# Kernel tuning notes

Hardware: AMD Instinct MI355X
Metric: run time of the kernel (lower is better)

## Reference

```python
import jax, jax.numpy as jnp
import numpy as np

NUM_HEADS = 16


def setup_inputs() -> dict:
    key = jax.random.key(0)
    ks = jax.random.split(key, 4)
    B, S, H = 2, 2048, 1024
    hidden_states = jax.random.normal(ks[0], (B, S, H), dtype=jnp.float32)
    attention_mask = jnp.zeros((B, 1, 1, S), dtype=jnp.float32)
    scale = 1.0 / np.sqrt(H)
    Wq = jax.random.normal(ks[1], (H, H), dtype=jnp.float32) * scale
    Wk = jax.random.normal(ks[2], (H, H), dtype=jnp.float32) * scale
    Wv = jax.random.normal(ks[3], (H, H), dtype=jnp.float32) * scale
    bq = jnp.zeros((H,), dtype=jnp.float32)
    bk = jnp.zeros((H,), dtype=jnp.float32)
    bv = jnp.zeros((H,), dtype=jnp.float32)
    return {"hidden_states": hidden_states, "attention_mask": attention_mask,
            "Wq": Wq, "bq": bq, "Wk": Wk, "bk": bk, "Wv": Wv, "bv": bv}


def _split_heads(x, B, S):
    # [B, S, H] -> [B, h, S, d]
    return x.reshape(B, S, NUM_HEADS, -1).transpose(0, 2, 1, 3)


def reference(hidden_states, attention_mask, Wq, bq, Wk, bk, Wv, bv):
    B, S, H = hidden_states.shape
    d = H // NUM_HEADS
    q = _split_heads(hidden_states @ Wq + bq, B, S)  # [B,h,S,d]
    k = _split_heads(hidden_states @ Wk + bk, B, S)
    v = _split_heads(hidden_states @ Wv + bv, B, S)

    scores = jnp.einsum('bhqd,bhkd->bhqk', q, k) / jnp.sqrt(jnp.float32(d))
    # causal mask: -inf strictly above diagonal, plus additive pad mask
    i = jnp.arange(S)[:, None]
    j = jnp.arange(S)[None, :]
    causal = jnp.where(j > i, -jnp.inf, 0.0).astype(scores.dtype)  # [S,S]
    scores = scores + attention_mask + causal[None, None, :, :]

    probs = jax.nn.softmax(scores, axis=-1)  # dropout prob = 0.0 -> identity
    context = jnp.einsum('bhqk,bhkd->bhqd', probs, v)  # [B,h,S,d]
    return context.transpose(0, 2, 1, 3).reshape(B, S, H)
```

## Files before the change

kernel.cpp:

```cpp
#include <hip/hip_runtime.h>

typedef __attribute__((ext_vector_type(4))) float f32x4;
typedef __attribute__((ext_vector_type(8))) short bf16x8;

__device__ __forceinline__ ushort f2bf(float f) {
  union { float f; unsigned u; } v; v.f = f;
  unsigned u = v.u;
  return (ushort)((u + 0x7fffu + ((u >> 16) & 1u)) >> 16);
}

__global__ __launch_bounds__(256) void cvt_x(const float* __restrict__ x,
                                             ushort* __restrict__ o) {
  int idx = blockIdx.x * 256 + threadIdx.x;
  float4 v = reinterpret_cast<const float4*>(x)[idx];
  ushort4 r;
  r.x = f2bf(v.x); r.y = f2bf(v.y); r.z = f2bf(v.z); r.w = f2bf(v.w);
  reinterpret_cast<ushort4*>(o)[idx] = r;
}

__global__ __launch_bounds__(256) void wtrans(const float* __restrict__ Wq,
                                              const float* __restrict__ Wk,
                                              const float* __restrict__ Wv,
                                              ushort* __restrict__ WT) {
  __shared__ ushort tile[64 * 65];
  int bx = blockIdx.x;
  int w = bx >> 8;
  int rem = bx & 255;
  int k0 = (rem >> 4) << 6;
  int n0 = (rem & 15) << 6;
  const float* W = (w == 0) ? Wq : (w == 1) ? Wk : Wv;
  int tid = threadIdx.x;
#pragma unroll
  for (int it = 0; it < 16; ++it) {
    int idx = tid + it * 256;
    int r = idx >> 6, c = idx & 63;
    tile[r * 65 + c] = f2bf(W[(k0 + r) * 1024 + n0 + c]);
  }
  __syncthreads();
#pragma unroll
  for (int it = 0; it < 16; ++it) {
    int idx = tid + it * 256;
    int r = idx >> 6, c = idx & 63;
    WT[w * 1048576 + (n0 + r) * 1024 + k0 + c] = tile[c * 65 + r];
  }
}

__global__ __launch_bounds__(256) void qkv_gemm(
    const ushort* __restrict__ Xb, const ushort* __restrict__ WT,
    const float* __restrict__ bq, const float* __restrict__ bk,
    const float* __restrict__ bv, ushort* __restrict__ Qb,
    ushort* __restrict__ Kb, ushort* __restrict__ VT) {
  __shared__ ushort Xs[128 * 72];
  __shared__ ushort Ws[128 * 72];
  int tid = threadIdx.x;
  int wave = tid >> 6, lane = tid & 63, g = lane >> 4, lr = lane & 15;
  int wr = wave >> 1, wc = wave & 1;
  int m0 = blockIdx.x << 7;
  int n0g = blockIdx.y << 7;
  f32x4 acc[4][4];
#pragma unroll
  for (int i = 0; i < 4; ++i)
#pragma unroll
    for (int j = 0; j < 4; ++j) { acc[i][j][0] = 0.f; acc[i][j][1] = 0.f; acc[i][j][2] = 0.f; acc[i][j][3] = 0.f; }

  for (int k0 = 0; k0 < 1024; k0 += 64) {
#pragma unroll
    for (int c = 0; c < 4; ++c) {
      int lin = tid + (c << 8);
      int row = lin >> 3, cc = lin & 7;
      *reinterpret_cast<uint4*>(&Xs[row * 72 + cc * 8]) =
          *reinterpret_cast<const uint4*>(&Xb[(m0 + row) * 1024 + k0 + cc * 8]);
      *reinterpret_cast<uint4*>(&Ws[row * 72 + cc * 8]) =
          *reinterpret_cast<const uint4*>(&WT[(n0g + row) * 1024 + k0 + cc * 8]);
    }
    __syncthreads();
#pragma unroll
    for (int ks = 0; ks < 2; ++ks) {
      bf16x8 a[4], b[4];
#pragma unroll
      for (int mi = 0; mi < 4; ++mi)
        a[mi] = *reinterpret_cast<const bf16x8*>(&Xs[(wr * 64 + mi * 16 + lr) * 72 + ks * 32 + g * 8]);
#pragma unroll
      for (int ni = 0; ni < 4; ++ni)
        b[ni] = *reinterpret_cast<const bf16x8*>(&Ws[(wc * 64 + ni * 16 + lr) * 72 + ks * 32 + g * 8]);
#pragma unroll
      for (int mi = 0; mi < 4; ++mi)
#pragma unroll
        for (int ni = 0; ni < 4; ++ni)
          acc[mi][ni] = __builtin_amdgcn_mfma_f32_16x16x32_bf16(a[mi], b[ni], acc[mi][ni], 0, 0, 0);
    }
    __syncthreads();
  }
  int which = n0g >> 10;
  const float* bias = (which == 0) ? bq : (which == 1) ? bk : bv;
  int nb = (n0g & 1023) + wc * 64;
#pragma unroll
  for (int ni = 0; ni < 4; ++ni) {
    int n = nb + ni * 16 + lr;
    float bb = bias[n];
    int hh = n >> 6, dd = n & 63;
#pragma unroll
    for (int mi = 0; mi < 4; ++mi) {
      int mbase = m0 + wr * 64 + mi * 16 + g * 4;
      int b_ = mbase >> 11, s = mbase & 2047;
      if (which == 2) {
        ushort4 v4;
        v4.x = f2bf(acc[mi][ni][0] + bb);
        v4.y = f2bf(acc[mi][ni][1] + bb);
        v4.z = f2bf(acc[mi][ni][2] + bb);
        v4.w = f2bf(acc[mi][ni][3] + bb);
        *reinterpret_cast<ushort4*>(&VT[((size_t)(b_ * 16 + hh) * 64 + dd) * 2048 + s]) = v4;
      } else {
        ushort* ob = (which == 0) ? Qb : Kb;
#pragma unroll
        for (int r = 0; r < 4; ++r)
          ob[((size_t)(b_ * 16 + hh) * 2048 + s + r) * 64 + dd] = f2bf(acc[mi][ni][r] + bb);
      }
    }
  }
}

struct QTState {
  f32x4 o[4];
  float m[4], l[4];
};

__device__ __forceinline__ void attn_process(
    const ushort* Ks, const ushort* VsT, ushort* Psw,
    const bf16x8& aq0, const bf16x8& aq1, QTState& st,
    int g, int lr, int qw, int kv0, bool diag, const float* mv) {
  f32x4 sc[4];
#pragma unroll
  for (int sub = 0; sub < 4; ++sub) {
    f32x4 s;
    s[0] = 0.f; s[1] = 0.f; s[2] = 0.f; s[3] = 0.f;
    bf16x8 bk0 = *reinterpret_cast<const bf16x8*>(&Ks[(sub * 16 + lr) * 72 + g * 8]);
    bf16x8 bk1 = *reinterpret_cast<const bf16x8*>(&Ks[(sub * 16 + lr) * 72 + 32 + g * 8]);
    s = __builtin_amdgcn_mfma_f32_16x16x32_bf16(aq0, bk0, s, 0, 0, 0);
    s = __builtin_amdgcn_mfma_f32_16x16x32_bf16(aq1, bk1, s, 0, 0, 0);
    int kk = kv0 + sub * 16 + lr;
#pragma unroll
    for (int r = 0; r < 4; ++r) {
      float v = s[r] * 0.125f + mv[sub];
      if (diag) {
        int q = qw + g * 4 + r;
        v = (kk > q) ? -__builtin_inff() : v;
      }
      s[r] = v;
    }
    sc[sub] = s;
  }
  float alpha[4];
#pragma unroll
  for (int r = 0; r < 4; ++r) {
    float tm = fmaxf(fmaxf(sc[0][r], sc[1][r]), fmaxf(sc[2][r], sc[3][r]));
    tm = fmaxf(tm, __shfl_xor(tm, 1));
    tm = fmaxf(tm, __shfl_xor(tm, 2));
    tm = fmaxf(tm, __shfl_xor(tm, 4));
    tm = fmaxf(tm, __shfl_xor(tm, 8));
    float nm = fmaxf(st.m[r], tm);
    float al = __expf(st.m[r] - nm);
    float rs = 0.f;
#pragma unroll
    for (int sub = 0; sub < 4; ++sub) {
      float p = __expf(sc[sub][r] - nm);
      sc[sub][r] = p;
      rs += p;
    }
    rs += __shfl_xor(rs, 1);
    rs += __shfl_xor(rs, 2);
    rs += __shfl_xor(rs, 4);
    rs += __shfl_xor(rs, 8);
    st.l[r] = st.l[r] * al + rs;
    st.m[r] = nm;
    alpha[r] = al;
#pragma unroll
    for (int sub = 0; sub < 4; ++sub)
      Psw[(g * 4 + r) * 72 + sub * 16 + lr] = f2bf(sc[sub][r]);
  }
#pragma unroll
  for (int ns = 0; ns < 4; ++ns) {
#pragma unroll
    for (int r = 0; r < 4; ++r) st.o[ns][r] *= alpha[r];
  }
#pragma unroll
  for (int kc = 0; kc < 2; ++kc) {
    bf16x8 pa = *reinterpret_cast<const bf16x8*>(&Psw[lr * 72 + kc * 32 + g * 8]);
#pragma unroll
    for (int ds_ = 0; ds_ < 4; ++ds_) {
      bf16x8 vb = *reinterpret_cast<const bf16x8*>(&VsT[(ds_ * 16 + lr) * 72 + kc * 32 + g * 8]);
      st.o[ds_] = __builtin_amdgcn_mfma_f32_16x16x32_bf16(pa, vb, st.o[ds_], 0, 0, 0);
    }
  }
}

__global__ __launch_bounds__(256) void attn(const ushort* __restrict__ Qb,
                                            const ushort* __restrict__ Kb,
                                            const ushort* __restrict__ VT,
                                            const float* __restrict__ mask,
                                            float* __restrict__ out) {
  __shared__ ushort Ks[64 * 72];
  __shared__ ushort VsT[64 * 72];
  __shared__ ushort Ps[4][16 * 72];
  int tid = threadIdx.x;
  int wave = tid >> 6, lane = tid & 63, g = lane >> 4, lr = lane & 15;
  int pi = blockIdx.x, bh = blockIdx.y;
  int b_ = bh >> 4, h = bh & 15;
  int qa_t = pi, qb_t = 31 - pi;
  const ushort* Qh = Qb + (size_t)bh * 2048 * 64;
  const ushort* Kh = Kb + (size_t)bh * 2048 * 64;
  const ushort* VTh = VT + (size_t)bh * 64 * 2048;
  int qa_w = qa_t * 64 + wave * 16;
  int qb_w = qb_t * 64 + wave * 16;

  bf16x8 aqa0 = *reinterpret_cast<const bf16x8*>(&Qh[(qa_w + lr) * 64 + g * 8]);
  bf16x8 aqa1 = *reinterpret_cast<const bf16x8*>(&Qh[(qa_w + lr) * 64 + 32 + g * 8]);
  bf16x8 aqb0 = *reinterpret_cast<const bf16x8*>(&Qh[(qb_w + lr) * 64 + g * 8]);
  bf16x8 aqb1 = *reinterpret_cast<const bf16x8*>(&Qh[(qb_w + lr) * 64 + 32 + g * 8]);

  QTState sa, sb;
#pragma unroll
  for (int i = 0; i < 4; ++i) {
    sa.o[i][0] = 0.f; sa.o[i][1] = 0.f; sa.o[i][2] = 0.f; sa.o[i][3] = 0.f;
    sb.o[i][0] = 0.f; sb.o[i][1] = 0.f; sb.o[i][2] = 0.f; sb.o[i][3] = 0.f;
    sa.m[i] = -__builtin_inff(); sa.l[i] = 0.f;
    sb.m[i] = -__builtin_inff(); sb.l[i] = 0.f;
  }
  ushort* Psw = Ps[wave];

  for (int t = 0; t <= qb_t; ++t) {
    int kv0 = t << 6;
#pragma unroll
    for (int c = 0; c < 2; ++c) {
      int lin = tid + (c << 8);
      int row = lin >> 3, cc = lin & 7;
      *reinterpret_cast<uint4*>(&Ks[row * 72 + cc * 8]) =
          *reinterpret_cast<const uint4*>(&Kh[(kv0 + row) * 64 + cc * 8]);
      *reinterpret_cast<uint4*>(&VsT[row * 72 + cc * 8]) =
          *reinterpret_cast<const uint4*>(&VTh[row * 2048 + kv0 + cc * 8]);
    }
    float mv[4];
#pragma unroll
    for (int sub = 0; sub < 4; ++sub) mv[sub] = mask[b_ * 2048 + kv0 + sub * 16 + lr];
    __syncthreads();
    if (t <= qa_t)
      attn_process(Ks, VsT, Psw, aqa0, aqa1, sa, g, lr, qa_w, kv0, t == qa_t, mv);
    attn_process(Ks, VsT, Psw, aqb0, aqb1, sb, g, lr, qb_w, kv0, t == qb_t, mv);
    __syncthreads();
  }

#pragma unroll
  for (int ns = 0; ns < 4; ++ns) {
#pragma unroll
    for (int r = 0; r < 4; ++r) {
      int qa = qa_w + g * 4 + r;
      out[(size_t)(b_ * 2048 + qa) * 1024 + h * 64 + ns * 16 + lr] = sa.o[ns][r] / sa.l[r];
      int qb = qb_w + g * 4 + r;
      out[(size_t)(b_ * 2048 + qb) * 1024 + h * 64 + ns * 16 + lr] = sb.o[ns][r] / sb.l[r];
    }
  }
}

extern "C" void kernel_launch(void* const* d_in, const int* in_sizes, int n_in,
                              void* d_out, int out_size, void* d_ws, size_t ws_size,
                              hipStream_t stream) {
  const float* X    = (const float*)d_in[0];
  const float* mask = (const float*)d_in[1];
  const float* Wq   = (const float*)d_in[2];
  const float* bq   = (const float*)d_in[3];
  const float* Wk   = (const float*)d_in[4];
  const float* bk   = (const float*)d_in[5];
  const float* Wv   = (const float*)d_in[6];
  const float* bv   = (const float*)d_in[7];
  float* out = (float*)d_out;

  char* ws = (char*)d_ws;
  ushort* Xb  = (ushort*)ws;
  ushort* WTb = (ushort*)(ws + 8388608);
  ushort* Qb  = (ushort*)(ws + 8388608 + 6291456);
  ushort* Kb  = Qb + 4194304;
  ushort* VT  = Kb + 4194304;

  cvt_x<<<4096, 256, 0, stream>>>(X, Xb);
  wtrans<<<768, 256, 0, stream>>>(Wq, Wk, Wv, WTb);
  qkv_gemm<<<dim3(32, 24), 256, 0, stream>>>(Xb, WTb, bq, bk, bv, Qb, Kb, VT);
  attn<<<dim3(16, 32), 256, 0, stream>>>(Qb, Kb, VT, mask, out);
}
```

Before: 218.4 us.

## Rewrite attention with 32x32 MFMA, register-resident P, and LDS-staged GEMM epilogue

The attention kernel now gives each wave 32 query rows, handled with 32x32x16 MFMAs in transposed form. The probabilities stay in registers via v_cvt_pk_bf16 and permlane32_swap instead of a round trip through LDS. It also swizzles K and V in LDS, skips the rescale when the max rises by less than a threshold, and stages the output through LDS for coalesced float4 stores. The QKV GEMM loads tiles with global_load_lds, uses setprio around its MFMAs, and writes its epilogue through LDS for vectorized stores. These changes target LDS traffic, bank conflicts and scattered stores, at the cost of more complexity and reliance on gfx950-specific instructions.

```diff
diff --git a/kernel.cpp b/kernel.cpp
--- a/kernel.cpp
+++ b/kernel.cpp
@@ -1,12 +1,29 @@
 #include <hip/hip_runtime.h>
 
-typedef __attribute__((ext_vector_type(4))) float f32x4;
-typedef __attribute__((ext_vector_type(8))) short bf16x8;
+typedef __attribute__((ext_vector_type(4)))  float f32x4;
+typedef __attribute__((ext_vector_type(16))) float f32x16;
+typedef __attribute__((ext_vector_type(8)))  short bf16x8;
+
+typedef __attribute__((address_space(1))) const void gvoid;
+typedef __attribute__((address_space(3))) void lvoid;
+
+__device__ __forceinline__ void gl_lds16(const void* g, void* l) {
+  __builtin_amdgcn_global_load_lds((gvoid*)g, (lvoid*)l, 16, 0, 0);
+}
 
 __device__ __forceinline__ ushort f2bf(float f) {
   union { float f; unsigned u; } v; v.f = f;
   unsigned u = v.u;
   return (ushort)((u + 0x7fffu + ((u >> 16) & 1u)) >> 16);
+}
+
+__device__ __forceinline__ uint cvt_pk_bf16(float lo, float hi) {
+  uint r;
+  asm("v_cvt_pk_bf16_f32 %0, %1, %2" : "=v"(r) : "v"(lo), "v"(hi));
+  return r;
+}
+__device__ __forceinline__ void plswap(uint& x, uint& y) {
+  asm volatile("v_permlane32_swap_b32 %0, %1" : "+v"(x), "+v"(y));
 }
 
 __global__ __launch_bounds__(256) void cvt_x(const float* __restrict__ x,
@@ -50,8 +67,9 @@
     const float* __restrict__ bq, const float* __restrict__ bk,
     const float* __restrict__ bv, ushort* __restrict__ Qb,
     ushort* __restrict__ Kb, ushort* __restrict__ VT) {
-  __shared__ ushort Xs[128 * 72];
-  __shared__ ushort Ws[128 * 72];
+  __shared__ ushort smem[128 * 136];
+  ushort* Xs = smem;
+  ushort* Ws = smem + 8192;
   int tid = threadIdx.x;
   int wave = tid >> 6, lane = tid & 63, g = lane >> 4, lr = lane & 15;
   int wr = wave >> 1, wc = wave & 1;
@@ -63,15 +81,15 @@
 #pragma unroll
     for (int j = 0; j < 4; ++j) { acc[i][j][0] = 0.f; acc[i][j][1] = 0.f; acc[i][j][2] = 0.f; acc[i][j][3] = 0.f; }
 
+  int lrow = lane >> 3, lcol = (lane & 7) * 8;
   for (int k0 = 0; k0 < 1024; k0 += 64) {
+    __syncthreads();
 #pragma unroll
     for (int c = 0; c < 4; ++c) {
-      int lin = tid + (c << 8);
-      int row = lin >> 3, cc = lin & 7;
-      *reinterpret_cast<uint4*>(&Xs[row * 72 + cc * 8]) =
-          *reinterpret_cast<const uint4*>(&Xb[(m0 + row) * 1024 + k0 + cc * 8]);
-      *reinterpret_cast<uint4*>(&Ws[row * 72 + cc * 8]) =
-          *reinterpret_cast<const uint4*>(&WT[(n0g + row) * 1024 + k0 + cc * 8]);
+      int cw = wave * 4 + c;
+      int row = cw * 8 + lrow;
+      gl_lds16(Xb + (size_t)(m0 + row) * 1024 + k0 + lcol, Xs + cw * 512);
+      gl_lds16(WT + (size_t)(n0g + row) * 1024 + k0 + lcol, Ws + cw * 512);
     }
     __syncthreads();
 #pragma unroll
@@ -79,117 +97,75 @@
       bf16x8 a[4], b[4];
 #pragma unroll
       for (int mi = 0; mi < 4; ++mi)
-        a[mi] = *reinterpret_cast<const bf16x8*>(&Xs[(wr * 64 + mi * 16 + lr) * 72 + ks * 32 + g * 8]);
+        a[mi] = *reinterpret_cast<const bf16x8*>(&Xs[(wr * 64 + mi * 16 + lr) * 64 + ks * 32 + g * 8]);
 #pragma unroll
       for (int ni = 0; ni < 4; ++ni)
-        b[ni] = *reinterpret_cast<const bf16x8*>(&Ws[(wc * 64 + ni * 16 + lr) * 72 + ks * 32 + g * 8]);
+        b[ni] = *reinterpret_cast<const bf16x8*>(&Ws[(wc * 64 + ni * 16 + lr) * 64 + ks * 32 + g * 8]);
+      __builtin_amdgcn_s_setprio(1);
 #pragma unroll
       for (int mi = 0; mi < 4; ++mi)
 #pragma unroll
         for (int ni = 0; ni < 4; ++ni)
           acc[mi][ni] = __builtin_amdgcn_mfma_f32_16x16x32_bf16(a[mi], b[ni], acc[mi][ni], 0, 0, 0);
-    }
-    __syncthreads();
-  }
+      __builtin_amdgcn_s_setprio(0);
+    }
+  }
+  __syncthreads();
+
   int which = n0g >> 10;
   const float* bias = (which == 0) ? bq : (which == 1) ? bk : bv;
-  int nb = (n0g & 1023) + wc * 64;
-#pragma unroll
-  for (int ni = 0; ni < 4; ++ni) {
-    int n = nb + ni * 16 + lr;
-    float bb = bias[n];
-    int hh = n >> 6, dd = n & 63;
-#pragma unroll
-    for (int mi = 0; mi < 4; ++mi) {
-      int mbase = m0 + wr * 64 + mi * 16 + g * 4;
-      int b_ = mbase >> 11, s = mbase & 2047;
-      if (which == 2) {
+  int nloc0 = (n0g & 1023);
+  if (which == 2) {
+#pragma unroll
+    for (int ni = 0; ni < 4; ++ni) {
+      int row = wc * 64 + ni * 16 + lr;
+      float bb = bias[nloc0 + row];
+#pragma unroll
+      for (int mi = 0; mi < 4; ++mi) {
+        int m = wr * 64 + mi * 16 + g * 4;
         ushort4 v4;
         v4.x = f2bf(acc[mi][ni][0] + bb);
         v4.y = f2bf(acc[mi][ni][1] + bb);
         v4.z = f2bf(acc[mi][ni][2] + bb);
         v4.w = f2bf(acc[mi][ni][3] + bb);
-        *reinterpret_cast<ushort4*>(&VT[((size_t)(b_ * 16 + hh) * 64 + dd) * 2048 + s]) = v4;
-      } else {
-        ushort* ob = (which == 0) ? Qb : Kb;
+        *reinterpret_cast<ushort4*>(&smem[row * 136 + m]) = v4;
+      }
+    }
+    __syncthreads();
+    int b_ = m0 >> 11, s0 = m0 & 2047;
+#pragma unroll
+    for (int it = 0; it < 8; ++it) {
+      int c = tid + it * 256;
+      int row = c >> 4, mc = (c & 15) * 8;
+      uint4 vv = *reinterpret_cast<const uint4*>(&smem[row * 136 + mc]);
+      int n = nloc0 + row;
+      int hh = n >> 6, dd = n & 63;
+      *reinterpret_cast<uint4*>(&VT[((size_t)(b_ * 16 + hh) * 64 + dd) * 2048 + s0 + mc]) = vv;
+    }
+  } else {
+#pragma unroll
+    for (int ni = 0; ni < 4; ++ni) {
+      int n = wc * 64 + ni * 16 + lr;
+      float bb = bias[nloc0 + n];
+#pragma unroll
+      for (int mi = 0; mi < 4; ++mi) {
 #pragma unroll
         for (int r = 0; r < 4; ++r)
-          ob[((size_t)(b_ * 16 + hh) * 2048 + s + r) * 64 + dd] = f2bf(acc[mi][ni][r] + bb);
-      }
-    }
-  }
-}
-
-struct QTState {
-  f32x4 o[4];
-  float m[4], l[4];
-};
-
-__device__ __forceinline__ void attn_process(
-    const ushort* Ks, const ushort* VsT, ushort* Psw,
-    const bf16x8& aq0, const bf16x8& aq1, QTState& st,
-    int g, int lr, int qw, int kv0, bool diag, const float* mv) {
-  f32x4 sc[4];
-#pragma unroll
-  for (int sub = 0; sub < 4; ++sub) {
-    f32x4 s;
-    s[0] = 0.f; s[1] = 0.f; s[2] = 0.f; s[3] = 0.f;
-    bf16x8 bk0 = *reinterpret_cast<const bf16x8*>(&Ks[(sub * 16 + lr) * 72 + g * 8]);
-    bf16x8 bk1 = *reinterpret_cast<const bf16x8*>(&Ks[(sub * 16 + lr) * 72 + 32 + g * 8]);
-    s = __builtin_amdgcn_mfma_f32_16x16x32_bf16(aq0, bk0, s, 0, 0, 0);
-    s = __builtin_amdgcn_mfma_f32_16x16x32_bf16(aq1, bk1, s, 0, 0, 0);
-    int kk = kv0 + sub * 16 + lr;
-#pragma unroll
-    for (int r = 0; r < 4; ++r) {
-      float v = s[r] * 0.125f + mv[sub];
-      if (diag) {
-        int q = qw + g * 4 + r;
-        v = (kk > q) ? -__builtin_inff() : v;
-      }
-      s[r] = v;
-    }
-    sc[sub] = s;
-  }
-  float alpha[4];
-#pragma unroll
-  for (int r = 0; r < 4; ++r) {
-    float tm = fmaxf(fmaxf(sc[0][r], sc[1][r]), fmaxf(sc[2][r], sc[3][r]));
-    tm = fmaxf(tm, __shfl_xor(tm, 1));
-    tm = fmaxf(tm, __shfl_xor(tm, 2));
-    tm = fmaxf(tm, __shfl_xor(tm, 4));
-    tm = fmaxf(tm, __shfl_xor(tm, 8));
-    float nm = fmaxf(st.m[r], tm);
-    float al = __expf(st.m[r] - nm);
-    float rs = 0.f;
-#pragma unroll
-    for (int sub = 0; sub < 4; ++sub) {
-      float p = __expf(sc[sub][r] - nm);
-      sc[sub][r] = p;
-      rs += p;
-    }
-    rs += __shfl_xor(rs, 1);
-    rs += __shfl_xor(rs, 2);
-    rs += __shfl_xor(rs, 4);
-    rs += __shfl_xor(rs, 8);
-    st.l[r] = st.l[r] * al + rs;
-    st.m[r] = nm;
-    alpha[r] = al;
-#pragma unroll
-    for (int sub = 0; sub < 4; ++sub)
-      Psw[(g * 4 + r) * 72 + sub * 16 + lr] = f2bf(sc[sub][r]);
-  }
-#pragma unroll
-  for (int ns = 0; ns < 4; ++ns) {
-#pragma unroll
-    for (int r = 0; r < 4; ++r) st.o[ns][r] *= alpha[r];
-  }
-#pragma unroll
-  for (int kc = 0; kc < 2; ++kc) {
-    bf16x8 pa = *reinterpret_cast<const bf16x8*>(&Psw[lr * 72 + kc * 32 + g * 8]);
-#pragma unroll
-    for (int ds_ = 0; ds_ < 4; ++ds_) {
-      bf16x8 vb = *reinterpret_cast<const bf16x8*>(&VsT[(ds_ * 16 + lr) * 72 + kc * 32 + g * 8]);
-      st.o[ds_] = __builtin_amdgcn_mfma_f32_16x16x32_bf16(pa, vb, st.o[ds_], 0, 0, 0);
+          smem[(wr * 64 + mi * 16 + g * 4 + r) * 136 + n] = f2bf(acc[mi][ni][r] + bb);
+      }
+    }
+    __syncthreads();
+    ushort* ob = (which == 0) ? Qb : Kb;
+#pragma unroll
+    for (int it = 0; it < 8; ++it) {
+      int c = tid + it * 256;
+      int row = c >> 4, nc = (c & 15) * 8;
+      uint4 vv = *reinterpret_cast<const uint4*>(&smem[row * 136 + nc]);
+      int m = m0 + row;
+      int b_ = m >> 11, s = m & 2047;
+      int n = nloc0 + nc;
+      int hh = n >> 6, dd = n & 63;
+      *reinterpret_cast<uint4*>(&ob[((size_t)(b_ * 16 + hh) * 2048 + s) * 64 + dd]) = vv;
     }
   }
 }
@@ -199,66 +175,155 @@
                                             const ushort* __restrict__ VT,
                                             const float* __restrict__ mask,
                                             float* __restrict__ out) {
-  __shared__ ushort Ks[64 * 72];
-  __shared__ ushort VsT[64 * 72];
-  __shared__ ushort Ps[4][16 * 72];
+  __shared__ char smem[34816];
+  ushort* Ks = (ushort*)smem;
+  ushort* Vs = (ushort*)(smem + 8192);
+  float*  Ms = (float*)(smem + 16384);
   int tid = threadIdx.x;
-  int wave = tid >> 6, lane = tid & 63, g = lane >> 4, lr = lane & 15;
-  int pi = blockIdx.x, bh = blockIdx.y;
+  int wave = tid >> 6, lane = tid & 63;
+  int hi = lane >> 5, l31 = lane & 31;
+  int pi = blockIdx.x & 15, bh = blockIdx.x >> 4;
   int b_ = bh >> 4, h = bh & 15;
-  int qa_t = pi, qb_t = 31 - pi;
   const ushort* Qh = Qb + (size_t)bh * 2048 * 64;
   const ushort* Kh = Kb + (size_t)bh * 2048 * 64;
   const ushort* VTh = VT + (size_t)bh * 64 * 2048;
-  int qa_w = qa_t * 64 + wave * 16;
-  int qb_w = qb_t * 64 + wave * 16;
-
-  bf16x8 aqa0 = *reinterpret_cast<const bf16x8*>(&Qh[(qa_w + lr) * 64 + g * 8]);
-  bf16x8 aqa1 = *reinterpret_cast<const bf16x8*>(&Qh[(qa_w + lr) * 64 + 32 + g * 8]);
-  bf16x8 aqb0 = *reinterpret_cast<const bf16x8*>(&Qh[(qb_w + lr) * 64 + g * 8]);
-  bf16x8 aqb1 = *reinterpret_cast<const bf16x8*>(&Qh[(qb_w + lr) * 64 + 32 + g * 8]);
-
-  QTState sa, sb;
-#pragma unroll
-  for (int i = 0; i < 4; ++i) {
-    sa.o[i][0] = 0.f; sa.o[i][1] = 0.f; sa.o[i][2] = 0.f; sa.o[i][3] = 0.f;
-    sb.o[i][0] = 0.f; sb.o[i][1] = 0.f; sb.o[i][2] = 0.f; sb.o[i][3] = 0.f;
-    sa.m[i] = -__builtin_inff(); sa.l[i] = 0.f;
-    sb.m[i] = -__builtin_inff(); sb.l[i] = 0.f;
-  }
-  ushort* Psw = Ps[wave];
-
-  for (int t = 0; t <= qb_t; ++t) {
+
+  int tile = (wave < 2) ? pi : (31 - pi);
+  int q0w = tile * 64 + (wave & 1) * 32;
+  int tmax = 31 - pi;
+
+  bf16x8 aq[4];
+#pragma unroll
+  for (int ds = 0; ds < 4; ++ds)
+    aq[ds] = *reinterpret_cast<const bf16x8*>(Qh + (q0w + l31) * 64 + ds * 16 + hi * 8);
+
+  f32x16 Od0, Od1;
+#pragma unroll
+  for (int j = 0; j < 16; ++j) { Od0[j] = 0.f; Od1[j] = 0.f; }
+  float mrun = -__builtin_inff(), lrun = 0.f;
+
+  for (int t = 0; t <= tmax; ++t) {
     int kv0 = t << 6;
+    __syncthreads();
 #pragma unroll
     for (int c = 0; c < 2; ++c) {
-      int lin = tid + (c << 8);
-      int row = lin >> 3, cc = lin & 7;
-      *reinterpret_cast<uint4*>(&Ks[row * 72 + cc * 8]) =
-          *reinterpret_cast<const uint4*>(&Kh[(kv0 + row) * 64 + cc * 8]);
-      *reinterpret_cast<uint4*>(&VsT[row * 72 + cc * 8]) =
-          *reinterpret_cast<const uint4*>(&VTh[row * 2048 + kv0 + cc * 8]);
-    }
-    float mv[4];
-#pragma unroll
-    for (int sub = 0; sub < 4; ++sub) mv[sub] = mask[b_ * 2048 + kv0 + sub * 16 + lr];
-    __syncthreads();
-    if (t <= qa_t)
-      attn_process(Ks, VsT, Psw, aqa0, aqa1, sa, g, lr, qa_w, kv0, t == qa_t, mv);
-    attn_process(Ks, VsT, Psw, aqb0, aqb1, sb, g, lr, qb_w, kv0, t == qb_t, mv);
-    __syncthreads();
-  }
-
-#pragma unroll
-  for (int ns = 0; ns < 4; ++ns) {
-#pragma unroll
-    for (int r = 0; r < 4; ++r) {
-      int qa = qa_w + g * 4 + r;
-      out[(size_t)(b_ * 2048 + qa) * 1024 + h * 64 + ns * 16 + lr] = sa.o[ns][r] / sa.l[r];
-      int qb = qb_w + g * 4 + r;
-      out[(size_t)(b_ * 2048 + qb) * 1024 + h * 64 + ns * 16 + lr] = sb.o[ns][r] / sb.l[r];
-    }
-  }
+      int ch = tid + (c << 8);
+      int row = ch >> 3, e0 = (ch & 7) * 8, bc = (ch & 7) << 4;
+      int sw = bc ^ ((row & 7) << 4);
+      uint4 kvv = *reinterpret_cast<const uint4*>(Kh + (size_t)(kv0 + row) * 64 + e0);
+      *reinterpret_cast<uint4*>((char*)Ks + row * 128 + sw) = kvv;
+      uint4 vvv = *reinterpret_cast<const uint4*>(VTh + (size_t)row * 2048 + kv0 + e0);
+      *reinterpret_cast<uint4*>((char*)Vs + row * 128 + sw) = vvv;
+    }
+    if (tid < 64) Ms[tid] = mask[b_ * 2048 + kv0 + tid];
+    __syncthreads();
+
+#pragma unroll
+    for (int sub = 0; sub < 2; ++sub) {
+      int kvb = kv0 + sub * 32;
+      if (kvb > q0w) continue;
+      bool dg = (kvb == q0w);
+
+      f32x16 s;
+#pragma unroll
+      for (int j = 0; j < 16; ++j) s[j] = 0.f;
+      __builtin_amdgcn_s_setprio(1);
+#pragma unroll
+      for (int ds = 0; ds < 4; ++ds) {
+        int krow = sub * 32 + l31;
+        bf16x8 kf = *reinterpret_cast<const bf16x8*>(
+            (char*)Ks + krow * 128 + ((ds * 32 + hi * 16) ^ ((krow & 7) << 4)));
+        s = __builtin_amdgcn_mfma_f32_32x32x16_bf16(kf, aq[ds], s, 0, 0, 0);
+      }
+      __builtin_amdgcn_s_setprio(0);
+
+#pragma unroll
+      for (int jj = 0; jj < 4; ++jj) {
+        float4 mv4 = *reinterpret_cast<const float4*>(Ms + sub * 32 + jj * 8 + 4 * hi);
+        const float* mvp = (const float*)&mv4;
+#pragma unroll
+        for (int r = 0; r < 4; ++r) {
+          int j = jj * 4 + r;
+          float sv = s[j] * 0.125f + mvp[r];
+          if (dg) {
+            int kvg = kvb + jj * 8 + 4 * hi + r;
+            sv = (kvg > q0w + l31) ? -__builtin_inff() : sv;
+          }
+          s[j] = sv;
+        }
+      }
+
+      float tmx = s[0];
+#pragma unroll
+      for (int j = 1; j < 16; ++j) tmx = fmaxf(tmx, s[j]);
+      tmx = fmaxf(tmx, __shfl_xor(tmx, 32));
+      bool defer = __all(tmx - mrun <= 8.0f);
+      float al = 1.0f;
+      if (!defer) {
+        float nm = fmaxf(mrun, tmx);
+        al = __expf(mrun - nm);
+        mrun = nm;
+      }
+      float rs = 0.f;
+#pragma unroll
+      for (int j = 0; j < 16; ++j) {
+        float p = __expf(s[j] - mrun);
+        s[j] = p;
+        rs += p;
+      }
+      rs += __shfl_xor(rs, 32);
+      lrun = lrun * al + rs;
+      if (!defer) {
+#pragma unroll
+        for (int j = 0; j < 16; ++j) { Od0[j] *= al; Od1[j] *= al; }
+      }
+
+      uint x0 = cvt_pk_bf16(s[0], s[1]),   y0 = cvt_pk_bf16(s[4], s[5]);
+      uint x1 = cvt_pk_bf16(s[2], s[3]),   y1 = cvt_pk_bf16(s[6], s[7]);
+      plswap(x0, y0); plswap(x1, y1);
+      uint x2 = cvt_pk_bf16(s[8], s[9]),   y2 = cvt_pk_bf16(s[12], s[13]);
+      uint x3 = cvt_pk_bf16(s[10], s[11]), y3 = cvt_pk_bf16(s[14], s[15]);
+      plswap(x2, y2); plswap(x3, y3);
+      union U { uint w[4]; bf16x8 v; };
+      U pa0, pa1;
+      pa0.w[0] = x0; pa0.w[1] = x1; pa0.w[2] = y0; pa0.w[3] = y1;
+      pa1.w[0] = x2; pa1.w[1] = x3; pa1.w[2] = y2; pa1.w[3] = y3;
+
+      __builtin_amdgcn_s_setprio(1);
+#pragma unroll
+      for (int ks = 0; ks < 2; ++ks) {
+        bf16x8 pf = ks ? pa1.v : pa0.v;
+        int bc = sub * 64 + ks * 32 + hi * 16;
+        int r0 = l31, r1 = 32 + l31;
+        bf16x8 v0 = *reinterpret_cast<const bf16x8*>((char*)Vs + r0 * 128 + (bc ^ ((r0 & 7) << 4)));
+        Od0 = __builtin_amdgcn_mfma_f32_32x32x16_bf16(v0, pf, Od0, 0, 0, 0);
+        bf16x8 v1 = *reinterpret_cast<const bf16x8*>((char*)Vs + r1 * 128 + (bc ^ ((r1 & 7) << 4)));
+        Od1 = __builtin_amdgcn_mfma_f32_32x32x16_bf16(v1, pf, Od1, 0, 0, 0);
+      }
+      __builtin_amdgcn_s_setprio(0);
+    }
+  }
+
+  __syncthreads();
+  float rl = 1.0f / lrun;
+  float* Ot = (float*)smem + wave * (32 * 68);
+#pragma unroll
+  for (int jj = 0; jj < 4; ++jj) {
+    int d0a = jj * 8 + 4 * hi;
+    float4 w0, w1;
+    w0.x = Od0[jj * 4 + 0] * rl; w0.y = Od0[jj * 4 + 1] * rl;
+    w0.z = Od0[jj * 4 + 2] * rl; w0.w = Od0[jj * 4 + 3] * rl;
+    w1.x = Od1[jj * 4 + 0] * rl; w1.y = Od1[jj * 4 + 1] * rl;
+    w1.z = Od1[jj * 4 + 2] * rl; w1.w = Od1[jj * 4 + 3] * rl;
+    *reinterpret_cast<float4*>(&Ot[l31 * 68 + d0a]) = w0;
+    *reinterpret_cast<float4*>(&Ot[l31 * 68 + 32 + d0a]) = w1;
+  }
+  int qr = lane >> 1, half = lane & 1;
+  const float* Orow = &Ot[qr * 68 + half * 32];
+  float* og = out + (size_t)(b_ * 2048 + q0w + qr) * 1024 + h * 64 + half * 32;
+#pragma unroll
+  for (int c2 = 0; c2 < 8; ++c2)
+    *reinterpret_cast<float4*>(og + c2 * 4) = *reinterpret_cast<const float4*>(Orow + c2 * 4);
 }
 
 extern "C" void kernel_launch(void* const* d_in, const int* in_sizes, int n_in,
@@ -284,5 +349,5 @@
   cvt_x<<<4096, 256, 0, stream>>>(X, Xb);
   wtrans<<<768, 256, 0, stream>>>(Wq, Wk, Wv, WTb);
   qkv_gemm<<<dim3(32, 24), 256, 0, stream>>>(Xb, WTb, bq, bk, bv, Qb, Kb, VT);
-  attn<<<dim3(16, 32), 256, 0, stream>>>(Qb, Kb, VT, mask, out);
-}
+  attn<<<512, 256, 0, stream>>>(Qb, Kb, VT, mask, out);
+}
```

Result: slower. 238.8 us (+9.3%).
